# Performance work log

Hardware: AMD Instinct MI355X
Metric: run time of the kernel (lower is better)

## Reference

```python
import jax, jax.numpy as jnp
import numpy as np

B, L, S, H, E = 2, 2048, 2048, 8, 64

def setup_inputs() -> dict:
    key = jax.random.key(0)
    k1, k2, k3 = jax.random.split(key, 3)
    queries = jax.random.normal(k1, (B, L, H, E), dtype=jnp.float32)
    keys = jax.random.normal(k2, (B, S, H, E), dtype=jnp.float32)
    values = jax.random.normal(k3, (B, S, H, E), dtype=jnp.float32)
    # TriangularCausalMask: True above the diagonal (positions to mask out)
    attn_mask = jnp.broadcast_to(
        jnp.triu(jnp.ones((L, S), dtype=bool), k=1)[None, None], (B, 1, L, S)
    )
    return {"queries": queries, "keys": keys, "values": values, "attn_mask": attn_mask}

def reference(queries, keys, values, attn_mask):
    E_ = queries.shape[-1]
    scale = 1.0 / (E_ ** 0.5)  # self.scale is None -> 1/sqrt(E)
    # scores: [B, H, L, S]
    scores = jnp.einsum('blhe,bshe->bhls', queries, keys)
    scores = jnp.where(attn_mask, -jnp.inf, scores)  # masked_fill_(mask, -inf)
    series = jax.nn.softmax(scale * scores, axis=-1)  # dropout p=0.0 -> identity
    V = jnp.einsum('bhls,bshd->blhd', series, values)
    return V, series
```

## Files before the change

kernel.cpp:

```cpp
#include <hip/hip_runtime.h>
#include <hip/hip_bf16.h>

typedef __attribute__((ext_vector_type(8))) short bf16x8;
typedef __attribute__((ext_vector_type(4))) short s16x4;
typedef __attribute__((ext_vector_type(4))) float f32x4;

constexpr int B = 2, L = 2048, S = 2048, H = 8, E = 64;
constexpr int TL = 64;
constexpr int SN = 64;
constexpr int LDK = 72;
constexpr int THREADS = 256;
constexpr int GSTR = H * E;

__device__ __forceinline__ float bf2f(short s) {
  union { unsigned u; float f; } c; c.u = ((unsigned)(unsigned short)s) << 16;
  return c.f;
}
__device__ __forceinline__ short f2bf(float x) {
  union { float f; unsigned u; } c; c.f = x;
  unsigned r = c.u + 0x7fffu + ((c.u >> 16) & 1u);
  return (short)(r >> 16);
}
__device__ __forceinline__ f32x4 mk4(float a, float b, float c, float d) {
  f32x4 v; v[0] = a; v[1] = b; v[2] = c; v[3] = d; return v;
}

struct Tile16 { f32x4 v0, v1, v2, v3; };

__device__ __forceinline__ void ld_tile(const float* __restrict__ g, int tid, Tile16& t) {
  const int r = tid >> 2, c = (tid & 3) * 16;
  const f32x4* q = (const f32x4*)(g + (size_t)r * GSTR + c);
  t.v0 = q[0]; t.v1 = q[1]; t.v2 = q[2]; t.v3 = q[3];
}

__device__ __forceinline__ void cvt_tile(const Tile16& t, short* __restrict__ o) {
  float vv[16] = { t.v0[0],t.v0[1],t.v0[2],t.v0[3], t.v1[0],t.v1[1],t.v1[2],t.v1[3],
                   t.v2[0],t.v2[1],t.v2[2],t.v2[3], t.v3[0],t.v3[1],t.v3[2],t.v3[3] };
#pragma unroll
  for (int k = 0; k < 8; ++k) {
    __hip_bfloat162 h = __float22bfloat162_rn(make_float2(vv[2*k], vv[2*k+1]));
    short2 s2 = *(short2*)&h;
    o[2*k] = s2.x; o[2*k+1] = s2.y;
  }
}

__device__ __forceinline__ void stK(const Tile16& t, short (* __restrict__ Kb)[LDK], int tid) {
  const int r = tid >> 2, c = (tid & 3) * 16;
  short s[16]; cvt_tile(t, s);
  *(bf16x8*)&Kb[r][c]     = *(bf16x8*)&s[0];
  *(bf16x8*)&Kb[r][c + 8] = *(bf16x8*)&s[8];
}

__device__ __forceinline__ void stV(const Tile16& t, short (* __restrict__ Vb)[LDK], int tid) {
  const int sr = tid >> 2, c = (tid & 3) * 16;
  short s[16]; cvt_tile(t, s);
#pragma unroll
  for (int i = 0; i < 16; ++i) {
    const int e = c + i;
    Vb[e][sr ^ (8 * ((e >> 3) & 7))] = s[i];
  }
}

__device__ __forceinline__ bf16x8 cvt8(f32x4 u0, f32x4 u1) {
  short o[8];
  float vv[8] = { u0[0],u0[1],u0[2],u0[3], u1[0],u1[1],u1[2],u1[3] };
#pragma unroll
  for (int k = 0; k < 4; ++k) {
    __hip_bfloat162 h = __float22bfloat162_rn(make_float2(vv[2*k], vv[2*k+1]));
    short2 s2 = *(short2*)&h;
    o[2*k] = s2.x; o[2*k+1] = s2.y;
  }
  return *(bf16x8*)o;
}

__device__ __forceinline__ int swz_t(int raw) {
  return (raw & 1) ? (31 - (raw >> 1)) : (raw >> 1);
}

__global__ __launch_bounds__(THREADS, 2)
void k_rowsum(const float* __restrict__ Q, const float* __restrict__ K,
              float* __restrict__ outV, float* __restrict__ outS,
              float* __restrict__ ws)
{
  __shared__ __align__(16) short Qs[TL][LDK];
  __shared__ __align__(16) short Ks[2][SN][LDK];

  const int tid  = threadIdx.x;
  const int lane = tid & 63;
  const int wv   = tid >> 6;
  const int quad = lane >> 4;
  const int n16  = lane & 15;

  const int t  = swz_t(blockIdx.x);
  const int bh = blockIdx.y;
  const int b = bh >> 3, h = bh & 7;
  const int l0 = t * TL;
  const int s_hi = l0 + TL;
  const int nt = s_hi / SN;

  const size_t qbase = ((size_t)b * L * H + h) * E;
  const size_t kbase = ((size_t)b * S * H + h) * E;
  const size_t srow  = (size_t)bh * L * S;

  {
    const f32x4 z = {0.f, 0.f, 0.f, 0.f};
#pragma unroll
    for (int i = 0; i < 4; ++i) {
      const int idx = tid * 4 + i;
      const int r = idx >> 4, c = idx & 15;
      *(f32x4*)(outV + qbase + (size_t)(l0 + r) * GSTR + c * 4) = z;
    }
  }

  {
    const f32x4 z = {0.f, 0.f, 0.f, 0.f};
    for (int r = 0; r < TL; ++r) {
      f32x4* p = (f32x4*)(outS + srow + (size_t)(l0 + r) * S);
      for (int s4 = s_hi / 4 + tid; s4 < S / 4; s4 += THREADS)
        __builtin_nontemporal_store(z, p + s4);
    }
  }

  Tile16 pk;
  ld_tile(K + kbase, tid, pk);
  {
    Tile16 tq;
    ld_tile(Q + qbase + (size_t)l0 * GSTR, tid, tq);
    stK(tq, Qs, tid);
  }
  __syncthreads();

  bf16x8 a0 = *(const bf16x8*)&Qs[wv * 16 + n16][quad * 8];
  bf16x8 a1 = *(const bf16x8*)&Qs[wv * 16 + n16][32 + quad * 8];

  float rsum[4] = {0.f, 0.f, 0.f, 0.f};
  for (int st = 0; st < nt; ++st) {
    short (*Kb)[LDK] = Ks[st & 1];
    stK(pk, Kb, tid);
    if (st + 1 < nt)
      ld_tile(K + kbase + (size_t)(st + 1) * SN * GSTR, tid, pk);
    __syncthreads();

    const int s0 = st * SN;
#pragma unroll
    for (int nn = 0; nn < 4; ++nn) {
      bf16x8 b0 = *(const bf16x8*)&Kb[nn * 16 + n16][quad * 8];
      bf16x8 b1 = *(const bf16x8*)&Kb[nn * 16 + n16][32 + quad * 8];
      f32x4 acc = {0.f, 0.f, 0.f, 0.f};
      acc = __builtin_amdgcn_mfma_f32_16x16x32_bf16(a0, b0, acc, 0, 0, 0);
      acc = __builtin_amdgcn_mfma_f32_16x16x32_bf16(a1, b1, acc, 0, 0, 0);
#pragma unroll
      for (int r = 0; r < 4; ++r) {
        const int l = l0 + wv * 16 + quad * 4 + r;
        const int s = s0 + nn * 16 + n16;
        rsum[r] += (s <= l) ? __expf(acc[r] * 0.125f) : 0.f;
      }
    }
    __syncthreads();
  }

#pragma unroll
  for (int r = 0; r < 4; ++r)
#pragma unroll
    for (int off = 1; off < 16; off <<= 1)
      rsum[r] += __shfl_xor(rsum[r], off, 64);
  if (n16 == 0)
#pragma unroll
    for (int r = 0; r < 4; ++r)
      ws[(size_t)bh * L + l0 + wv * 16 + quad * 4 + r] = 1.f / rsum[r];
}

__global__ __launch_bounds__(THREADS, 3)
void k_pv(const float* __restrict__ Q, const float* __restrict__ K,
          const float* __restrict__ V, float* __restrict__ outV,
          float* __restrict__ outS, const float* __restrict__ ws)
{
  __shared__ __align__(16) short Ks[2][SN][LDK];
  __shared__ __align__(16) short Vt[2][E][LDK];
  __shared__ __align__(16) short Ps[4][16][LDK];

  const int tid  = threadIdx.x;
  const int lane = tid & 63;
  const int wv   = tid >> 6;
  const int quad = lane >> 4;
  const int n16  = lane & 15;

  const int t  = swz_t(blockIdx.x >> 1);
  const int hh = blockIdx.x & 1;
  const int bh = blockIdx.y;
  const int b = bh >> 3, h = bh & 7;
  const int l0 = t * TL;
  const int nt = (l0 + TL) / SN;
  const int st0 = hh ? (nt + 1) / 2 : 0;
  const int st1 = hh ? nt : (nt + 1) / 2;

  const size_t qbase = ((size_t)b * L * H + h) * E;
  const size_t kbase = ((size_t)b * S * H + h) * E;
  const size_t srow  = (size_t)bh * L * S;

  const int qrow = l0 + wv * 16 + n16;
  const float* qp = Q + qbase + (size_t)qrow * GSTR;
  bf16x8 a0 = cvt8(*(const f32x4*)(qp + quad * 8), *(const f32x4*)(qp + quad * 8 + 4));
  bf16x8 a1 = cvt8(*(const f32x4*)(qp + 32 + quad * 8), *(const f32x4*)(qp + 36 + quad * 8));

  float inv_r[4];
#pragma unroll
  for (int r = 0; r < 4; ++r)
    inv_r[r] = ws[(size_t)bh * L + l0 + wv * 16 + quad * 4 + r];

  f32x4 oacc[4] = {{0,0,0,0},{0,0,0,0},{0,0,0,0},{0,0,0,0}};

  Tile16 pk2, pv2;
  if (st0 < st1) {
    ld_tile(K + kbase + (size_t)st0 * SN * GSTR, tid, pk2);
    ld_tile(V + kbase + (size_t)st0 * SN * GSTR, tid, pv2);
  }

  for (int st = st0; st < st1; ++st) {
    const int s0 = st * SN;
    const int buf = (st - st0) & 1;
    short (*Kb)[LDK] = Ks[buf];
    short (*Vb)[LDK] = Vt[buf];
    stK(pk2, Kb, tid);
    stV(pv2, Vb, tid);
    if (st + 1 < st1) {
      ld_tile(K + kbase + (size_t)(st + 1) * SN * GSTR, tid, pk2);
      ld_tile(V + kbase + (size_t)(st + 1) * SN * GSTR, tid, pv2);
    }
    __syncthreads();

#pragma unroll
    for (int nn = 0; nn < 4; ++nn) {
      bf16x8 b0 = *(const bf16x8*)&Kb[nn * 16 + n16][quad * 8];
      bf16x8 b1 = *(const bf16x8*)&Kb[nn * 16 + n16][32 + quad * 8];
      f32x4 acc = {0.f, 0.f, 0.f, 0.f};
      acc = __builtin_amdgcn_mfma_f32_16x16x32_bf16(a0, b0, acc, 0, 0, 0);
      acc = __builtin_amdgcn_mfma_f32_16x16x32_bf16(a1, b1, acc, 0, 0, 0);
#pragma unroll
      for (int r = 0; r < 4; ++r) {
        const int l = l0 + wv * 16 + quad * 4 + r;
        const int s = s0 + nn * 16 + n16;
        float w = (s <= l) ? __expf(acc[r] * 0.125f) * inv_r[r] : 0.f;
        Ps[wv][quad * 4 + r][(nn * 16 + n16) ^ (8 * quad)] = f2bf(w);
      }
    }

    asm volatile("s_waitcnt lgkmcnt(0)" ::: "memory");

    {
      const int row = lane >> 2;
      const int sub = lane & 3;
      const int swz = 8 * (lane >> 4);
      float* dstrow = outS + srow + (size_t)(l0 + wv * 16 + row) * S + s0;
#pragma unroll
      for (int i = 0; i < 4; ++i) {
        const int c = (i * 16 + sub * 4) ^ swz;
        s16x4 pw = *(const s16x4*)&Ps[wv][row][c];
        f32x4 o = mk4(bf2f(pw[0]), bf2f(pw[1]), bf2f(pw[2]), bf2f(pw[3]));
        __builtin_nontemporal_store(o, (f32x4*)(dstrow + i * 16 + sub * 4));
      }
    }

    {
      const int psw = 8 * ((n16 >> 2) & 3);
      bf16x8 pa0 = *(const bf16x8*)&Ps[wv][n16][(quad * 8)      ^ psw];
      bf16x8 pa1 = *(const bf16x8*)&Ps[wv][n16][(32 + quad * 8) ^ psw];
#pragma unroll
      for (int nn = 0; nn < 4; ++nn) {
        const int e   = nn * 16 + n16;
        const int vsw = 8 * ((e >> 3) & 7);
        bf16x8 vb0 = *(const bf16x8*)&Vb[e][(quad * 8)      ^ vsw];
        bf16x8 vb1 = *(const bf16x8*)&Vb[e][(32 + quad * 8) ^ vsw];
        oacc[nn] = __builtin_amdgcn_mfma_f32_16x16x32_bf16(pa0, vb0, oacc[nn], 0, 0, 0);
        oacc[nn] = __builtin_amdgcn_mfma_f32_16x16x32_bf16(pa1, vb1, oacc[nn], 0, 0, 0);
      }
    }
    __syncthreads();
  }

#pragma unroll
  for (int nn = 0; nn < 4; ++nn)
#pragma unroll
    for (int r = 0; r < 4; ++r) {
      const int l = l0 + wv * 16 + quad * 4 + r;
      atomicAdd(&outV[qbase + (size_t)l * GSTR + nn * 16 + n16], oacc[nn][r]);
    }
}

extern "C" void kernel_launch(void* const* d_in, const int* in_sizes, int n_in,
                              void* d_out, int out_size, void* d_ws, size_t ws_size,
                              hipStream_t stream) {
  const float* Q = (const float*)d_in[0];
  const float* K = (const float*)d_in[1];
  const float* V = (const float*)d_in[2];
  float* outV = (float*)d_out;
  float* outS = outV + (size_t)B * L * H * E;
  float* inv  = (float*)d_ws;
  k_rowsum<<<dim3(L / TL, B * H), THREADS, 0, stream>>>(Q, K, outV, outS, inv);
  k_pv<<<dim3(2 * L / TL, B * H), THREADS, 0, stream>>>(Q, K, V, outV, outS, inv);
}
```

Baseline: 388.1 us.

## Split rowsum kernel over two KV halves and PV kernel into four parts

The row-sum kernel now launches twice as many blocks. Each block covers half of the causal key tiles and half of the zero-fill work, and writes partial sums to two workspace slots. The PV kernel splits each query tile's key range into four parts instead of two, and combines the two partial row sums into the reciprocal at load time. The aim is more parallelism and less tail imbalance on the long causal rows, at the cost of more atomicAdds into the output and more redundant Q loads.

```diff
diff --git a/kernel.cpp b/kernel.cpp
--- a/kernel.cpp
+++ b/kernel.cpp
@@ -91,12 +91,15 @@
   const int quad = lane >> 4;
   const int n16  = lane & 15;
 
-  const int t  = swz_t(blockIdx.x);
+  const int t  = swz_t(blockIdx.x >> 1);
+  const int hh = blockIdx.x & 1;
   const int bh = blockIdx.y;
   const int b = bh >> 3, h = bh & 7;
   const int l0 = t * TL;
   const int s_hi = l0 + TL;
   const int nt = s_hi / SN;
+  const int st0 = hh ? (nt + 1) / 2 : 0;
+  const int st1 = hh ? nt : (nt + 1) / 2;
 
   const size_t qbase = ((size_t)b * L * H + h) * E;
   const size_t kbase = ((size_t)b * S * H + h) * E;
@@ -105,24 +108,29 @@
   {
     const f32x4 z = {0.f, 0.f, 0.f, 0.f};
 #pragma unroll
-    for (int i = 0; i < 4; ++i) {
-      const int idx = tid * 4 + i;
-      const int r = idx >> 4, c = idx & 15;
+    for (int i = 0; i < 2; ++i) {
+      const int idx = tid * 2 + i;
+      const int r = (idx >> 4) + hh * 32, c = idx & 15;
       *(f32x4*)(outV + qbase + (size_t)(l0 + r) * GSTR + c * 4) = z;
     }
   }
 
   {
+    const int s4lo = s_hi / 4;
+    const int mid  = s4lo + (((S / 4 - s4lo) >> 1) & ~15);
+    const int lo = hh ? mid : s4lo;
+    const int hi = hh ? S / 4 : mid;
     const f32x4 z = {0.f, 0.f, 0.f, 0.f};
     for (int r = 0; r < TL; ++r) {
       f32x4* p = (f32x4*)(outS + srow + (size_t)(l0 + r) * S);
-      for (int s4 = s_hi / 4 + tid; s4 < S / 4; s4 += THREADS)
+      for (int s4 = lo + tid; s4 < hi; s4 += THREADS)
         __builtin_nontemporal_store(z, p + s4);
     }
   }
 
   Tile16 pk;
-  ld_tile(K + kbase, tid, pk);
+  if (st0 < st1)
+    ld_tile(K + kbase + (size_t)st0 * SN * GSTR, tid, pk);
   {
     Tile16 tq;
     ld_tile(Q + qbase + (size_t)l0 * GSTR, tid, tq);
@@ -134,10 +142,10 @@
   bf16x8 a1 = *(const bf16x8*)&Qs[wv * 16 + n16][32 + quad * 8];
 
   float rsum[4] = {0.f, 0.f, 0.f, 0.f};
-  for (int st = 0; st < nt; ++st) {
-    short (*Kb)[LDK] = Ks[st & 1];
+  for (int st = st0; st < st1; ++st) {
+    short (*Kb)[LDK] = Ks[(st - st0) & 1];
     stK(pk, Kb, tid);
-    if (st + 1 < nt)
+    if (st + 1 < st1)
       ld_tile(K + kbase + (size_t)(st + 1) * SN * GSTR, tid, pk);
     __syncthreads();
 
@@ -167,7 +175,7 @@
   if (n16 == 0)
 #pragma unroll
     for (int r = 0; r < 4; ++r)
-      ws[(size_t)bh * L + l0 + wv * 16 + quad * 4 + r] = 1.f / rsum[r];
+      ws[(size_t)(hh * B * H + bh) * L + l0 + wv * 16 + quad * 4 + r] = rsum[r];
 }
 
 __global__ __launch_bounds__(THREADS, 3)
@@ -185,14 +193,15 @@
   const int quad = lane >> 4;
   const int n16  = lane & 15;
 
-  const int t  = swz_t(blockIdx.x >> 1);
-  const int hh = blockIdx.x & 1;
+  const int t    = swz_t(blockIdx.x >> 2);
+  const int part = blockIdx.x & 3;
   const int bh = blockIdx.y;
   const int b = bh >> 3, h = bh & 7;
   const int l0 = t * TL;
   const int nt = (l0 + TL) / SN;
-  const int st0 = hh ? (nt + 1) / 2 : 0;
-  const int st1 = hh ? nt : (nt + 1) / 2;
+  const int st0 = (part * nt) >> 2;
+  const int st1 = ((part + 1) * nt) >> 2;
+  if (st0 >= st1) return;
 
   const size_t qbase = ((size_t)b * L * H + h) * E;
   const size_t kbase = ((size_t)b * S * H + h) * E;
@@ -205,16 +214,16 @@
 
   float inv_r[4];
 #pragma unroll
-  for (int r = 0; r < 4; ++r)
-    inv_r[r] = ws[(size_t)bh * L + l0 + wv * 16 + quad * 4 + r];
+  for (int r = 0; r < 4; ++r) {
+    const size_t idx = (size_t)l0 + wv * 16 + quad * 4 + r;
+    inv_r[r] = 1.f / (ws[(size_t)bh * L + idx] + ws[(size_t)(B * H + bh) * L + idx]);
+  }
 
   f32x4 oacc[4] = {{0,0,0,0},{0,0,0,0},{0,0,0,0},{0,0,0,0}};
 
   Tile16 pk2, pv2;
-  if (st0 < st1) {
-    ld_tile(K + kbase + (size_t)st0 * SN * GSTR, tid, pk2);
-    ld_tile(V + kbase + (size_t)st0 * SN * GSTR, tid, pv2);
-  }
+  ld_tile(K + kbase + (size_t)st0 * SN * GSTR, tid, pk2);
+  ld_tile(V + kbase + (size_t)st0 * SN * GSTR, tid, pv2);
 
   for (int st = st0; st < st1; ++st) {
     const int s0 = st * SN;
@@ -296,6 +305,6 @@
   float* outV = (float*)d_out;
   float* outS = outV + (size_t)B * L * H * E;
   float* inv  = (float*)d_ws;
-  k_rowsum<<<dim3(L / TL, B * H), THREADS, 0, stream>>>(Q, K, outV, outS, inv);
-  k_pv<<<dim3(2 * L / TL, B * H), THREADS, 0, stream>>>(Q, K, V, outV, outS, inv);
-}
+  k_rowsum<<<dim3(2 * L / TL, B * H), THREADS, 0, stream>>>(Q, K, outV, outS, inv);
+  k_pv<<<dim3(4 * L / TL, B * H), THREADS, 0, stream>>>(Q, K, V, outV, outS, inv);
+}
```

Measured after the change: 390.4 us. No clear change (+0.6%).
